# Performance work log

Hardware: AMD Instinct MI355X
Metric: run time of the kernel (lower is better)

Reference implementation:

```python
import jax, jax.numpy as jnp
import numpy as np
from jax import lax

K_NEIGHBORS = 8  # num_neighbors
EPS_BN = 1e-5

def _bn(x, g, b, axes):
    # training-mode batch norm over `axes`, channel axis = 1
    m = jnp.mean(x, axis=axes, keepdims=True)
    v = jnp.var(x, axis=axes, keepdims=True)
    shp = [1] * x.ndim; shp[1] = x.shape[1]
    return (x - m) / jnp.sqrt(v + EPS_BN) * g.reshape(shp) + b.reshape(shp)

def _conv(x, w, b):
    y = lax.conv_general_dilated(x, w, (1, 1), 'SAME',
                                 dimension_numbers=('NCHW', 'OIHW', 'NCHW'))
    return y + b[None, :, None, None]

def setup_inputs() -> dict:
    key = jax.random.key(0)
    ks = jax.random.split(key, 20)
    B, C, H, W = 64, 200, 27, 27
    D, F, NC, HID = 64, 9, 16, 128
    inp = {
        'x': jax.random.normal(ks[0], (B, C, H, W), jnp.float32),
        'conv1_w': jax.random.normal(ks[1], (32, C, 3, 3), jnp.float32) * 0.02,
        'conv1_b': jnp.zeros((32,), jnp.float32),
        'bn1_g': jnp.ones((32,), jnp.float32), 'bn1_b': jnp.zeros((32,), jnp.float32),
        'conv2_w': jax.random.normal(ks[2], (64, 32, 3, 3), jnp.float32) * 0.05,
        'conv2_b': jnp.zeros((64,), jnp.float32),
        'bn2_g': jnp.ones((64,), jnp.float32), 'bn2_b': jnp.zeros((64,), jnp.float32),
        'conv3_w': jax.random.normal(ks[3], (D, 64, 3, 3), jnp.float32) * 0.05,
        'conv3_b': jnp.zeros((D,), jnp.float32),
        'bn3_g': jnp.ones((D,), jnp.float32), 'bn3_b': jnp.zeros((D,), jnp.float32),
        'w_self': jax.random.normal(ks[4], (D, D), jnp.float32) * (2.0 / (2 * D)) ** 0.5,
        'w_nb': jax.random.normal(ks[5], (D, D), jnp.float32) * (2.0 / (2 * D)) ** 0.5,
        'gkan_bias': jnp.zeros((D,), jnp.float32),
        'kan_a': jax.random.normal(ks[6], (D, 3), jnp.float32) * 0.1,
        'kan_b': jax.random.normal(ks[7], (D, 2), jnp.float32) * 0.1,
        'gkan_bn_g': jnp.ones((D,), jnp.float32), 'gkan_bn_b': jnp.zeros((D,), jnp.float32),
        'centers': jax.random.normal(ks[8], (D, F), jnp.float32),
        'gamma': jnp.ones((D, F), jnp.float32) * 0.5,
        'attn_w1': jax.random.normal(ks[9], (D // 4, D), jnp.float32) * 0.1,
        'attn_b1': jnp.zeros((D // 4,), jnp.float32),
        'attn_w2': jax.random.normal(ks[10], (D, D // 4), jnp.float32) * 0.1,
        'attn_b2': jnp.zeros((D,), jnp.float32),
        'fa_bn_g': jnp.ones((D,), jnp.float32), 'fa_bn_b': jnp.zeros((D,), jnp.float32),
        'fc1_w': jax.random.normal(ks[11], (HID, D), jnp.float32) * 0.1,
        'fc1_b': jnp.zeros((HID,), jnp.float32),
        'cls_bn_g': jnp.ones((HID,), jnp.float32), 'cls_bn_b': jnp.zeros((HID,), jnp.float32),
        'fc2_w': jax.random.normal(ks[12], (NC, HID), jnp.float32) * 0.1,
        'fc2_b': jnp.zeros((NC,), jnp.float32),
    }
    return inp

def _forward(x, conv1_w, conv1_b, bn1_g, bn1_b, conv2_w, conv2_b, bn2_g, bn2_b,
             conv3_w, conv3_b, bn3_g, bn3_b, w_self, w_nb, gkan_bias, kan_a, kan_b,
             gkan_bn_g, gkan_bn_b, centers, gamma, attn_w1, attn_b1, attn_w2, attn_b2,
             fa_bn_g, fa_bn_b, fc1_w, fc1_b, cls_bn_g, cls_bn_b, fc2_w, fc2_b):
    # --- CNN encoder ---
    h = jax.nn.relu(_bn(_conv(x, conv1_w, conv1_b), bn1_g, bn1_b, (0, 2, 3)))
    h = jax.nn.relu(_bn(_conv(h, conv2_w, conv2_b), bn2_g, bn2_b, (0, 2, 3)))
    h = jax.nn.relu(_bn(_conv(h, conv3_w, conv3_b), bn3_g, bn3_b, (0, 2, 3)))
    # --- tokenize: [B,D,H,W] -> [B,N,D] ---
    B, D, H, W = h.shape
    N = H * W
    t = h.reshape(B, D, N).transpose(0, 2, 1)
    # --- kNN graph (vectorized topk + scatter) ---
    xx = jnp.sum(t * t, axis=-1, keepdims=True)               # [B,N,1]
    xy = jnp.einsum('bnd,bmd->bnm', t, t)                     # [B,N,N]
    dist = jnp.maximum(xx - 2.0 * xy + xx.transpose(0, 2, 1), 0.0)
    k = min(K_NEIGHBORS + 1, N)
    _, idx = lax.top_k(-dist, k)                              # smallest-k, [B,N,k]
    adj = jnp.zeros((B, N, N), t.dtype).at[
        jnp.arange(B)[:, None, None], jnp.arange(N)[None, :, None], idx[:, :, 1:]
    ].set(1.0)
    deg = jnp.sum(adj, axis=-1) + 1e-6                        # [B,N]
    dinv = deg ** -0.5
    adj_norm = dinv[:, :, None] * adj * dinv[:, None, :] + jnp.eye(N, dtype=t.dtype)[None]
    # --- GKAN graph conv ---
    h_self = t @ w_self                                       # [B,N,D]
    h_nb = jnp.einsum('bnm,bmd->bnd', adj_norm, t @ w_nb)
    g = h_self + h_nb + gkan_bias
    g2 = g * g
    num = kan_a[:, 0] + kan_a[:, 1] * g + kan_a[:, 2] * g2
    den = 1.0 + jnp.abs(kan_b[:, 0] * g + kan_b[:, 1] * g2)
    g = num / (den + 1e-8)
    g = _bn(g.transpose(0, 2, 1), gkan_bn_g, gkan_bn_b, (0, 2)).transpose(0, 2, 1)
    # --- Fuzzy attention (RBF membership; logsumexp(log(v+1e-10)) == sum(v+1e-10)) ---
    d2 = (g[..., None] - centers[None, None]) ** 2            # [B,N,D,F]
    rbf = jnp.sum(jnp.exp(-jnp.abs(gamma)[None, None] * d2) + 1e-10, axis=-1)
    a1 = jax.nn.relu(rbf @ attn_w1.T + attn_b1)
    attn = jax.nn.sigmoid(a1 @ attn_w2.T + attn_b2)
    g = g * attn + g
    g = _bn(g.transpose(0, 2, 1), fa_bn_g, fa_bn_b, (0, 2)).transpose(0, 2, 1)
    # dropout: identity in eval
    # --- global pool + classifier ---
    p = 0.5 * jnp.mean(g, axis=1) + 0.5 * jnp.max(g, axis=1)  # [B,D]
    c = p @ fc1_w.T + fc1_b
    c = jax.nn.relu(_bn(c, cls_bn_g, cls_bn_b, (0,)))
    return c @ fc2_w.T + fc2_b

def reference(x, conv1_w, conv1_b, bn1_g, bn1_b, conv2_w, conv2_b, bn2_g, bn2_b,
              conv3_w, conv3_b, bn3_g, bn3_b, w_self, w_nb, gkan_bias, kan_a, kan_b,
              gkan_bn_g, gkan_bn_b, centers, gamma, attn_w1, attn_b1, attn_w2, attn_b2,
              fa_bn_g, fa_bn_b, fc1_w, fc1_b, cls_bn_g, cls_bn_b, fc2_w, fc2_b):
    return _forward(x, conv1_w, conv1_b, bn1_g, bn1_b, conv2_w, conv2_b, bn2_g, bn2_b,
                    conv3_w, conv3_b, bn3_g, bn3_b, w_self, w_nb, gkan_bias, kan_a, kan_b,
                    gkan_bn_g, gkan_bn_b, centers, gamma, attn_w1, attn_b1, attn_w2, attn_b2,
                    fa_bn_g, fa_bn_b, fc1_w, fc1_b, cls_bn_g, cls_bn_b, fc2_w, fc2_b)
```

## Files before the change

### kernel.cpp

```cpp
#include <hip/hip_runtime.h>
#include <math.h>

#define BATCH 64
#define NTOK  729
#define DIM   64
#define NROWS 46656

#define SROW 33
#define SCH  (29 * SROW)

template<int CIN_CHUNK, bool BN_IN>
__global__ __launch_bounds__(256) void conv3x3_v4(
    const float* __restrict__ in, const float* __restrict__ wgt,
    const float* __restrict__ scsh, float* __restrict__ outp,
    int Cin, int Cout, int cinPerSlab, int nslab)
{
  int bigGroups = Cout / 16;
  int blocksPerB = bigGroups * nslab;
  int b = blockIdx.x / blocksPerB;
  int rr = blockIdx.x % blocksPerB;
  int bg = rr / nslab;
  int slab = rr % nslab;
  int c_begin = slab * cinPerSlab;
  int c_end = c_begin + cinPerSlab; if (c_end > Cin) c_end = Cin;

  __shared__ float s_in[CIN_CHUNK * SCH + SROW];
  __shared__ float s_w[16 * CIN_CHUNK * 12];
  __shared__ float s_sc[CIN_CHUNK];
  __shared__ float s_sh[CIN_CHUNK];

  const int tid = threadIdx.x;
  const int grp = tid >> 7;
  const int idx = tid & 127;
  const bool active = idx < 126;
  const int rp = idx / 9;
  const int py = 2 * rp;
  const int px3 = (idx % 9) * 3;
  const bool row2ok = (py + 1) < 27;

  float acc[8][2][3];
  #pragma unroll
  for (int t = 0; t < 8; ++t)
    #pragma unroll
    for (int rI = 0; rI < 2; ++rI) { acc[t][rI][0]=0.f; acc[t][rI][1]=0.f; acc[t][rI][2]=0.f; }

  const size_t inB = (size_t)b * Cin;

  for (int c0 = c_begin; c0 < c_end; c0 += CIN_CHUNK) {
    int ccn = c_end - c0; if (ccn > CIN_CHUNK) ccn = CIN_CHUNK;
    if (BN_IN && tid < ccn) {
      s_sc[tid] = scsh[c0 + tid];
      s_sh[tid] = scsh[Cin + c0 + tid];
    }
    __syncthreads();
    for (int i = tid; i < CIN_CHUNK * SCH; i += 256) {
      int cc = i / SCH; int r2 = i - cc * SCH; int y = r2 / SROW; int x2 = r2 - y * SROW;
      float v = 0.f;
      if (cc < ccn && y >= 1 && y <= 27 && x2 >= 1 && x2 <= 27) {
        v = in[(inB + (c0 + cc)) * 729 + (y - 1) * 27 + (x2 - 1)];
        if (BN_IN) v = fmaxf(fmaf(v, s_sc[cc], s_sh[cc]), 0.f);
      }
      s_in[i] = v;
    }
    for (int i = tid; i < 16 * CIN_CHUNK * 9; i += 256) {
      int t = i / (CIN_CHUNK * 9); int r2 = i - t * CIN_CHUNK * 9;
      int cc = r2 / 9; int k = r2 - cc * 9;
      float wv = 0.f;
      if (cc < ccn) wv = wgt[((size_t)(bg * 16 + t) * Cin + (c0 + cc)) * 9 + k];
      s_w[(t * CIN_CHUNK + cc) * 12 + k] = wv;
    }
    __syncthreads();
    if (active) {
      #pragma unroll 1
      for (int cc = 0; cc < ccn; ++cc) {
        const float* bp = &s_in[cc * SCH + py * SROW + px3];
        float r0[5], r1[5], r2[5], r3[5];
        #pragma unroll
        for (int j = 0; j < 5; ++j) {
          r0[j] = bp[j];
          r1[j] = bp[SROW + j];
          r2[j] = bp[2*SROW + j];
          r3[j] = bp[3*SROW + j];
        }
        #pragma unroll
        for (int t = 0; t < 8; ++t) {
          const int wb = ((grp * 8 + t) * CIN_CHUNK + cc) * 12;
          const float4 wa = *(const float4*)&s_w[wb];
          const float4 wc = *(const float4*)&s_w[wb + 4];
          const float  w8 = s_w[wb + 8];
          #pragma unroll
          for (int p = 0; p < 3; ++p) {
            acc[t][0][p] += wa.x*r0[p]+wa.y*r0[p+1]+wa.z*r0[p+2]
                          + wa.w*r1[p]+wc.x*r1[p+1]+wc.y*r1[p+2]
                          + wc.z*r2[p]+wc.w*r2[p+1]+w8*r2[p+2];
            acc[t][1][p] += wa.x*r1[p]+wa.y*r1[p+1]+wa.z*r1[p+2]
                          + wa.w*r2[p]+wc.x*r2[p+1]+wc.y*r2[p+2]
                          + wc.z*r3[p]+wc.w*r3[p+1]+w8*r3[p+2];
          }
        }
      }
    }
  }
  if (active) {
    #pragma unroll
    for (int t = 0; t < 8; ++t) {
      size_t base = (((size_t)slab * BATCH + b) * Cout + (bg * 16 + grp * 8 + t)) * 729 + py * 27 + px3;
      outp[base+0]=acc[t][0][0]; outp[base+1]=acc[t][0][1]; outp[base+2]=acc[t][0][2];
      if (row2ok) {
        outp[base+27]=acc[t][1][0]; outp[base+28]=acc[t][1][1]; outp[base+29]=acc[t][1][2];
      }
    }
  }
}

__global__ __launch_bounds__(256) void conv_reduce_stats(
    const float* __restrict__ part, const float* __restrict__ bias,
    float* __restrict__ outp, double* __restrict__ stats, int C, int nslab)
{
  int b = blockIdx.x / C;
  int c = blockIdx.x % C;
  size_t slabStride = (size_t)BATCH * C * 729;
  size_t base = ((size_t)b * C + c) * 729;
  float bv = bias[c];
  float bsum = 0.f, bsq = 0.f;
  for (int e = threadIdx.x; e < 729; e += 256) {
    float v = bv;
    for (int s = 0; s < nslab; ++s) v += part[s*slabStride + base + e];
    outp[base + e] = v;
    bsum += v; bsq += v*v;
  }
  #pragma unroll
  for (int off = 32; off > 0; off >>= 1) {
    bsum += __shfl_down(bsum, off);
    bsq  += __shfl_down(bsq, off);
  }
  __shared__ float rs[4], rq[4];
  int wid = threadIdx.x >> 6;
  if ((threadIdx.x & 63) == 0) { rs[wid] = bsum; rq[wid] = bsq; }
  __syncthreads();
  if (threadIdx.x == 0) {
    float s1 = rs[0]+rs[1]+rs[2]+rs[3];
    float q1 = rq[0]+rq[1]+rq[2]+rq[3];
    atomicAdd(&stats[c], (double)s1);
    atomicAdd(&stats[C + c], (double)q1);
  }
}

__global__ void bn_finalize(const double* __restrict__ stats,
                            const float* __restrict__ gamma, const float* __restrict__ beta,
                            float* __restrict__ scsh, int C, float invCount)
{
  int c = threadIdx.x + blockIdx.x * blockDim.x; if (c >= C) return;
  double mu = stats[c] * (double)invCount;
  double var = stats[C + c] * (double)invCount - mu * mu;
  float rstd = (float)(1.0 / sqrt(var + 1e-5));
  float sc = gamma[c] * rstd;
  scsh[c] = sc;
  scsh[C + c] = beta[c] - (float)mu * sc;
}

__global__ __launch_bounds__(256) void bn_transpose_xx(
    const float* __restrict__ c3, const float* __restrict__ scsh,
    float* __restrict__ t, float* __restrict__ xx)
{
  int lb = (blockIdx.x & 7) * 96 + (blockIdx.x >> 3);
  int b = lb / 12, nt = lb % 12, n0 = nt * 64;
  __shared__ float s[64 * 65];
  for (int i = threadIdx.x; i < 4096; i += 256) {
    int d = i >> 6, j = i & 63; int n = n0 + j;
    float v = 0.f;
    if (n < 729) {
      v = c3[((size_t)b * 64 + d) * 729 + n];
      v = fmaxf(fmaf(v, scsh[d], scsh[64 + d]), 0.f);
    }
    s[d * 65 + j] = v;
  }
  __syncthreads();
  for (int i = threadIdx.x; i < 4096; i += 256) {
    int j = i >> 6, d = i & 63; int n = n0 + j;
    if (n < 729) t[((size_t)b * 729 + n) * 64 + d] = s[d * 65 + j];
  }
  if (threadIdx.x < 64) {
    int j = threadIdx.x; int n = n0 + j;
    if (n < 729) {
      float sm = 0.f;
      #pragma unroll
      for (int d = 0; d < 64; ++d) { float v = s[d * 65 + j]; sm += v * v; }
      xx[b * 729 + n] = sm;
    }
  }
}

__global__ __launch_bounds__(256) void gemm_selfnb(
    const float* __restrict__ t, const float* __restrict__ wself,
    const float* __restrict__ wnb, float* __restrict__ hs, float* __restrict__ hw)
{
  int lb = (blockIdx.x & 7) * 96 + (blockIdx.x >> 3);
  int b = lb / 12, nt = lb % 12, n0 = nt * 64;
  __shared__ __align__(16) float s_tT[64 * 68];
  __shared__ __align__(16) float s_a[64 * 68];
  __shared__ __align__(16) float s_b[64 * 68];
  const int tid = threadIdx.x;
  for (int i = tid; i < 1024; i += 256) {
    int n = i >> 4, dq = i & 15;
    float4 v = make_float4(0.f, 0.f, 0.f, 0.f);
    if (n0 + n < 729) v = *(const float4*)&t[((size_t)b * 729 + n0 + n) * 64 + 4 * dq];
    s_tT[(4*dq+0)*68 + n] = v.x;
    s_tT[(4*dq+1)*68 + n] = v.y;
    s_tT[(4*dq+2)*68 + n] = v.z;
    s_tT[(4*dq+3)*68 + n] = v.w;
  }
  for (int i = tid; i < 1024; i += 256) {
    int d = i >> 4, jq = i & 15;
    *(float4*)&s_a[d*68 + 4*jq] = *(const float4*)&wself[d*64 + 4*jq];
    *(float4*)&s_b[d*68 + 4*jq] = *(const float4*)&wnb[d*64 + 4*jq];
  }
  __syncthreads();
  int ty = tid >> 4, tx = tid & 15;
  float acc0[4][4], acc1[4][4];
  #pragma unroll
  for (int i = 0; i < 4; ++i)
    #pragma unroll
    for (int j = 0; j < 4; ++j) { acc0[i][j] = 0.f; acc1[i][j] = 0.f; }
  #pragma unroll 8
  for (int d = 0; d < 64; ++d) {
    float4 av = *(const float4*)&s_tT[d*68 + 4*ty];
    float4 b1 = *(const float4*)&s_a[d*68 + 4*tx];
    float4 b2 = *(const float4*)&s_b[d*68 + 4*tx];
    float a[4] = {av.x, av.y, av.z, av.w};
    float u[4] = {b1.x, b1.y, b1.z, b1.w};
    float w[4] = {b2.x, b2.y, b2.z, b2.w};
    #pragma unroll
    for (int i = 0; i < 4; ++i)
      #pragma unroll
      for (int j = 0; j < 4; ++j) { acc0[i][j] += a[i]*u[j]; acc1[i][j] += a[i]*w[j]; }
  }
  #pragma unroll
  for (int i = 0; i < 4; ++i) {
    int n = n0 + 4*ty + i;
    if (n < 729) {
      size_t o = ((size_t)b * 729 + n) * 64 + 4*tx;
      *(float4*)&hs[o] = make_float4(acc0[i][0], acc0[i][1], acc0[i][2], acc0[i][3]);
      *(float4*)&hw[o] = make_float4(acc1[i][0], acc1[i][1], acc1[i][2], acc1[i][3]);
    }
  }
}

__global__ __launch_bounds__(256) void dist_topk(
    const float* __restrict__ t, const float* __restrict__ xx, int* __restrict__ nbr)
{
  int lb = (blockIdx.x & 7) * 96 + (blockIdx.x >> 3);
  int b = lb / 12, nt = lb % 12, n0 = nt * 64;
  __shared__ __align__(16) float s_nT[64 * 68];
  __shared__ __align__(16) float s_mT[64 * 68];
  __shared__ __align__(16) float s_S[64 * 68];

  const int tid = threadIdx.x;
  const int ty = tid >> 4, tx = tid & 15;
  const int r = tid & 63, q = tid >> 6;
  const int n_self = n0 + r;
  const size_t tb = (size_t)b * 729;

  float kv[8]; int ki[8];
  #pragma unroll
  for (int i = 0; i < 8; ++i) { kv[i] = 3.0e38f; ki[i] = 0x7fffffff; }

  for (int i = tid; i < 1024; i += 256) {
    int n = i >> 4, dq = i & 15;
    float4 v = make_float4(0.f, 0.f, 0.f, 0.f);
    if (n0 + n < 729) v = *(const float4*)&t[(tb + n0 + n) * 64 + 4 * dq];
    s_nT[(4*dq+0)*68 + n] = v.x;
    s_nT[(4*dq+1)*68 + n] = v.y;
    s_nT[(4*dq+2)*68 + n] = v.z;
    s_nT[(4*dq+3)*68 + n] = v.w;
  }
  for (int i = tid; i < 1024; i += 256) {
    int m = i >> 4, dq = i & 15;
    float4 v = *(const float4*)&t[(tb + m) * 64 + 4 * dq];
    s_mT[(4*dq+0)*68 + m] = v.x;
    s_mT[(4*dq+1)*68 + m] = v.y;
    s_mT[(4*dq+2)*68 + m] = v.z;
    s_mT[(4*dq+3)*68 + m] = v.w;
  }
  __syncthreads();

  for (int mt = 0; mt < 12; ++mt) {
    int m0 = mt * 64;
    float acc[4][4];
    #pragma unroll
    for (int i = 0; i < 4; ++i)
      #pragma unroll
      for (int j = 0; j < 4; ++j) acc[i][j] = 0.f;
    #pragma unroll 8
    for (int d = 0; d < 64; ++d) {
      float4 av4 = *(const float4*)&s_nT[d*68 + 4*ty];
      float4 bv4 = *(const float4*)&s_mT[d*68 + 4*tx];
      float a[4] = {av4.x, av4.y, av4.z, av4.w};
      float bb[4] = {bv4.x, bv4.y, bv4.z, bv4.w};
      #pragma unroll
      for (int i = 0; i < 4; ++i)
        #pragma unroll
        for (int j = 0; j < 4; ++j) acc[i][j] += a[i] * bb[j];
    }
    float xm[4];
    #pragma unroll
    for (int j = 0; j < 4; ++j) {
      int m = m0 + 4*tx + j;
      xm[j] = (m < 729) ? xx[b * 729 + m] : 3.0e38f;
    }
    #pragma unroll
    for (int i = 0; i < 4; ++i) {
      float4 sc = make_float4(fmaf(-2.f, acc[i][0], xm[0]), fmaf(-2.f, acc[i][1], xm[1]),
                              fmaf(-2.f, acc[i][2], xm[2]), fmaf(-2.f, acc[i][3], xm[3]));
      *(float4*)&s_S[(4*ty + i)*68 + 4*tx] = sc;
    }
    __syncthreads();
    if (mt < 11) {
      int m0n = (mt + 1) * 64;
      for (int i = tid; i < 1024; i += 256) {
        int m = i >> 4, dq = i & 15;
        float4 v = make_float4(0.f, 0.f, 0.f, 0.f);
        if (m0n + m < 729) v = *(const float4*)&t[(tb + m0n + m) * 64 + 4 * dq];
        s_mT[(4*dq+0)*68 + m] = v.x;
        s_mT[(4*dq+1)*68 + m] = v.y;
        s_mT[(4*dq+2)*68 + m] = v.z;
        s_mT[(4*dq+3)*68 + m] = v.w;
      }
    }
    #pragma unroll
    for (int c = 0; c < 4; ++c) {
      float4 s4 = *(const float4*)&s_S[r*68 + q*16 + 4*c];
      float sv[4] = {s4.x, s4.y, s4.z, s4.w};
      #pragma unroll
      for (int k = 0; k < 4; ++k) {
        int m = m0 + q*16 + 4*c + k;
        bool valid = (m < 729) && (m != n_self);
        bool lt = valid && ((sv[k] < kv[7]) || (sv[k] == kv[7] && m < ki[7]));
        if (lt) {
          float cv = sv[k]; int ci = m;
          #pragma unroll
          for (int ii = 0; ii < 8; ++ii) {
            bool less = (cv < kv[ii]) || (cv == kv[ii] && ci < ki[ii]);
            float tv = less ? kv[ii] : cv; int ti = less ? ki[ii] : ci;
            kv[ii] = less ? cv : kv[ii]; ki[ii] = less ? ci : ki[ii];
            cv = tv; ci = ti;
          }
        }
      }
    }
    __syncthreads();
  }
  float* mv = s_mT;
  int*   mi = (int*)s_nT;
  #pragma unroll
  for (int i2 = 0; i2 < 8; ++i2) { mv[r*33 + q*8 + i2] = kv[i2]; mi[r*33 + q*8 + i2] = ki[i2]; }
  __syncthreads();
  if (tid < 64) {
    int n = n0 + tid;
    if (n < 729) {
      int rb = tid * 33;
      int p0 = 0, p1 = 0, p2 = 0, p3 = 0;
      int* op = &nbr[((size_t)b * 729 + n) * 8];
      for (int o = 0; o < 8; ++o) {
        float bvv = 3.5e38f; int bii = 0x7fffffff; int bq = 0;
        {
          float v = mv[rb + 0*8 + p0]; int ii = mi[rb + 0*8 + p0];
          if (v < bvv || (v == bvv && ii < bii)) { bvv = v; bii = ii; bq = 0; }
        }
        {
          float v = mv[rb + 1*8 + p1]; int ii = mi[rb + 1*8 + p1];
          if (v < bvv || (v == bvv && ii < bii)) { bvv = v; bii = ii; bq = 1; }
        }
        {
          float v = mv[rb + 2*8 + p2]; int ii = mi[rb + 2*8 + p2];
          if (v < bvv || (v == bvv && ii < bii)) { bvv = v; bii = ii; bq = 2; }
        }
        {
          float v = mv[rb + 3*8 + p3]; int ii = mi[rb + 3*8 + p3];
          if (v < bvv || (v == bvv && ii < bii)) { bvv = v; bii = ii; bq = 3; }
        }
        p0 += (bq == 0); p1 += (bq == 1); p2 += (bq == 2); p3 += (bq == 3);
        op[o] = bii;
      }
    }
  }
}

__global__ __launch_bounds__(256) void gkan_kernel(
    const float* __restrict__ hs, const float* __restrict__ hw,
    const int* __restrict__ nbr, const float* __restrict__ bias,
    const float* __restrict__ kan_a, const float* __restrict__ kan_b,
    float* __restrict__ gpre)
{
  int row = blockIdx.x * 4 + (threadIdx.x >> 6);
  int d = threadIdx.x & 63;
  float degf = 8.0f + 1e-6f;
  float coef = 1.0f / degf;
  size_t bbase = (size_t)(row / 729) * 729;
  float v = hs[(size_t)row * 64 + d] + hw[(size_t)row * 64 + d] + bias[d];
  float nsum = 0.f;
  #pragma unroll
  for (int j = 0; j < 8; ++j) {
    int m = nbr[(size_t)row * 8 + j];
    nsum += hw[(bbase + m) * 64 + d];
  }
  v += coef * nsum;
  float a0 = kan_a[d*3], a1 = kan_a[d*3+1], a2 = kan_a[d*3+2];
  float b0 = kan_b[d*2], b1 = kan_b[d*2+1];
  float v2 = v * v;
  float num = a0 + a1*v + a2*v2;
  float den = 1.f + fabsf(b0*v + b1*v2);
  gpre[(size_t)row * 64 + d] = num / (den + 1e-8f);
}

__global__ __launch_bounds__(256) void stats_tok(
    const float* __restrict__ g, double* __restrict__ stats)
{
  int d = threadIdx.x & 63, qq = threadIdx.x >> 6;
  int r0 = blockIdx.x * 183;
  int rend = r0 + 183; if (rend > NROWS) rend = NROWS;
  float sm = 0.f, sq = 0.f;
  for (int r = r0 + qq; r < rend; r += 4) {
    float v = g[(size_t)r * 64 + d];
    sm += v; sq += v * v;
  }
  __shared__ float ls[256], lq[256];
  ls[threadIdx.x] = sm; lq[threadIdx.x] = sq;
  __syncthreads();
  if (threadIdx.x < 64) {
    sm = ls[d] + ls[64+d] + ls[128+d] + ls[192+d];
    sq = lq[d] + lq[64+d] + lq[128+d] + lq[192+d];
    atomicAdd(&stats[d], (double)sm);
    atomicAdd(&stats[64 + d], (double)sq);
  }
}

__global__ __launch_bounds__(256) void fuzzy_attn(
    const float* __restrict__ gpre, const float* __restrict__ scshG,
    const float* __restrict__ centers, const float* __restrict__ gam,
    const float* __restrict__ w1, const float* __restrict__ b1,
    const float* __restrict__ w2, const float* __restrict__ b2,
    float* __restrict__ g2)
{
  int wv = threadIdx.x >> 6, d = threadIdx.x & 63;
  int row = blockIdx.x * 4 + wv;
  __shared__ float s_rbf[4][64];
  __shared__ float s_a1[4][16];
  float v = gpre[(size_t)row * 64 + d];
  float gn = fmaf(v, scshG[d], scshG[64 + d]);
  float acc = 0.f;
  #pragma unroll
  for (int f = 0; f < 9; ++f) {
    float dc = gn - centers[d*9 + f];
    acc += expf(-fabsf(gam[d*9 + f]) * dc * dc);
  }
  s_rbf[wv][d] = acc + 9e-10f;
  __syncthreads();
  if (d < 16) {
    float a = b1[d];
    #pragma unroll 8
    for (int k = 0; k < 64; ++k) a += w1[d*64 + k] * s_rbf[wv][k];
    s_a1[wv][d] = fmaxf(a, 0.f);
  }
  __syncthreads();
  float a2 = b2[d];
  #pragma unroll
  for (int i = 0; i < 16; ++i) a2 += w2[d*16 + i] * s_a1[wv][i];
  float sig = 1.f / (1.f + expf(-a2));
  g2[(size_t)row * 64 + d] = gn * (1.f + sig);
}

__global__ __launch_bounds__(256) void pool_kernel(
    const float* __restrict__ g2, const float* __restrict__ scshF, float* __restrict__ p)
{
  int b = blockIdx.x;
  int d = threadIdx.x & 63, qq = threadIdx.x >> 6;
  float sc = scshF[d], sh = scshF[64 + d];
  float sm = 0.f, mx = -3.0e38f;
  for (int n = qq; n < 729; n += 4) {
    float v = fmaf(g2[((size_t)b * 729 + n) * 64 + d], sc, sh);
    sm += v; mx = fmaxf(mx, v);
  }
  __shared__ float ls[256], lm[256];
  ls[threadIdx.x] = sm; lm[threadIdx.x] = mx;
  __syncthreads();
  if (threadIdx.x < 64) {
    sm = ls[d] + ls[64+d] + ls[128+d] + ls[192+d];
    mx = fmaxf(fmaxf(lm[d], lm[64+d]), fmaxf(lm[128+d], lm[192+d]));
    p[b * 64 + d] = 0.5f * (sm / 729.f) + 0.5f * mx;
  }
}

__global__ __launch_bounds__(256) void classifier(
    const float* __restrict__ p, const float* __restrict__ f1w, const float* __restrict__ f1b,
    const float* __restrict__ bng, const float* __restrict__ bnb,
    const float* __restrict__ f2w, const float* __restrict__ f2b, float* __restrict__ outp)
{
  __shared__ float s_p[64 * 64];
  __shared__ float s_c[64 * 128];
  __shared__ float s_sc[128], s_sh[128];
  for (int i = threadIdx.x; i < 4096; i += 256) s_p[i] = p[i];
  __syncthreads();
  for (int o = threadIdx.x; o < 8192; o += 256) {
    int b = o >> 7, h = o & 127;
    float acc = f1b[h];
    #pragma unroll 8
    for (int d = 0; d < 64; ++d) acc += s_p[b*64 + d] * f1w[h*64 + d];
    s_c[o] = acc;
  }
  __syncthreads();
  if (threadIdx.x < 128) {
    int h = threadIdx.x;
    float sm = 0.f, sq = 0.f;
    for (int b = 0; b < 64; ++b) { float v = s_c[b*128 + h]; sm += v; sq += v*v; }
    float mu = sm / 64.f;
    float var = sq / 64.f - mu * mu;
    float rstd = rsqrtf(var + 1e-5f);
    float sc = bng[h] * rstd;
    s_sc[h] = sc; s_sh[h] = bnb[h] - mu * sc;
  }
  __syncthreads();
  for (int o = threadIdx.x; o < 1024; o += 256) {
    int b = o >> 4, j = o & 15;
    float acc = f2b[j];
    #pragma unroll 8
    for (int h = 0; h < 128; ++h) {
      float v = fmaxf(fmaf(s_c[b*128 + h], s_sc[h], s_sh[h]), 0.f);
      acc += f2w[j*128 + h] * v;
    }
    outp[o] = acc;
  }
}

extern "C" void kernel_launch(void* const* d_in, const int* in_sizes, int n_in,
                              void* d_out, int out_size, void* d_ws, size_t ws_size,
                              hipStream_t stream)
{
  const float* x      = (const float*)d_in[0];
  const float* c1w    = (const float*)d_in[1];
  const float* c1b    = (const float*)d_in[2];
  const float* bn1g   = (const float*)d_in[3];
  const float* bn1b   = (const float*)d_in[4];
  const float* c2wt   = (const float*)d_in[5];
  const float* c2b    = (const float*)d_in[6];
  const float* bn2g   = (const float*)d_in[7];
  const float* bn2b   = (const float*)d_in[8];
  const float* c3wt   = (const float*)d_in[9];
  const float* c3b    = (const float*)d_in[10];
  const float* bn3g   = (const float*)d_in[11];
  const float* bn3b   = (const float*)d_in[12];
  const float* wself  = (const float*)d_in[13];
  const float* wnb    = (const float*)d_in[14];
  const float* gbias  = (const float*)d_in[15];
  const float* kana   = (const float*)d_in[16];
  const float* kanb   = (const float*)d_in[17];
  const float* gbng   = (const float*)d_in[18];
  const float* gbnb   = (const float*)d_in[19];
  const float* cent   = (const float*)d_in[20];
  const float* gamr   = (const float*)d_in[21];
  const float* aw1    = (const float*)d_in[22];
  const float* ab1    = (const float*)d_in[23];
  const float* aw2    = (const float*)d_in[24];
  const float* ab2    = (const float*)d_in[25];
  const float* fbng   = (const float*)d_in[26];
  const float* fbnb   = (const float*)d_in[27];
  const float* f1w    = (const float*)d_in[28];
  const float* f1b    = (const float*)d_in[29];
  const float* cbng   = (const float*)d_in[30];
  const float* cbnb   = (const float*)d_in[31];
  const float* f2w    = (const float*)d_in[32];
  const float* f2b    = (const float*)d_in[33];

  char* ws = (char*)d_ws;
  float*  P     = (float*) (ws + 0);
  float*  c1    = (float*) (ws + 23887872);
  float*  c2    = (float*) (ws + 29859840);
  float*  c3    = (float*) (ws + 41803776);
  int*    nbr   = (int*)   (ws + 53747712);
  float*  xx    = (float*) (ws + 55240704);
  double* stats = (double*)(ws + 55427328);
  float*  scsh  = (float*) (ws + 55431936);
  float*  pbuf  = (float*) (ws + 55434240);
  float* hw   = P;
  float* t    = (float*)(ws + 11943936);
  float* hs   = c2;
  float* gpre = c3;
  float* g2   = t;

  hipMemsetAsync(stats, 0, 576 * sizeof(double), stream);

  const float inv = 1.0f / 46656.0f;

  conv3x3_v4<8,false><<<dim3(512), dim3(256), 0, stream>>>(
      x,  c1w, nullptr, P, 200, 32, 50, 4);
  conv_reduce_stats<<<dim3(2048), dim3(256), 0, stream>>>(P, c1b, c1, stats, 32, 4);
  bn_finalize<<<dim3(1), dim3(32), 0, stream>>>(stats, bn1g, bn1b, scsh, 32, inv);
  conv3x3_v4<8,true><<<dim3(512), dim3(256), 0, stream>>>(
      c1, c2wt, scsh, P, 32, 64, 16, 2);
  conv_reduce_stats<<<dim3(4096), dim3(256), 0, stream>>>(P, c2b, c2, stats + 64, 64, 2);
  bn_finalize<<<dim3(1), dim3(64), 0, stream>>>(stats + 64, bn2g, bn2b, scsh + 64, 64, inv);
  conv3x3_v4<8,true><<<dim3(512), dim3(256), 0, stream>>>(
      c2, c3wt, scsh + 64, P, 64, 64, 32, 2);
  conv_reduce_stats<<<dim3(4096), dim3(256), 0, stream>>>(P, c3b, c3, stats + 192, 64, 2);
  bn_finalize<<<dim3(1), dim3(64), 0, stream>>>(stats + 192, bn3g, bn3b, scsh + 192, 64, inv);
  bn_transpose_xx<<<dim3(768), dim3(256), 0, stream>>>(c3, scsh + 192, t, xx);
  gemm_selfnb<<<dim3(768), dim3(256), 0, stream>>>(t, wself, wnb, hs, hw);
  dist_topk<<<dim3(768), dim3(256), 0, stream>>>(t, xx, nbr);
  gkan_kernel<<<dim3(11664), dim3(256), 0, stream>>>(hs, hw, nbr, gbias, kana, kanb, gpre);
  stats_tok<<<dim3(256), dim3(256), 0, stream>>>(gpre, stats + 320);
  bn_finalize<<<dim3(1), dim3(64), 0, stream>>>(stats + 320, gbng, gbnb, scsh + 320, 64, inv);
  fuzzy_attn<<<dim3(11664), dim3(256), 0, stream>>>(gpre, scsh + 320, cent, gamr, aw1, ab1, aw2, ab2, g2);
  stats_tok<<<dim3(256), dim3(256), 0, stream>>>(g2, stats + 448);
  bn_finalize<<<dim3(1), dim3(64), 0, stream>>>(stats + 448, fbng, fbnb, scsh + 448, 64, inv);
  pool_kernel<<<dim3(64), dim3(256), 0, stream>>>(g2, scsh + 448, pbuf);
  classifier<<<dim3(1), dim3(256), 0, stream>>>(pbuf, f1w, f1b, cbng, cbnb, f2w, f2b, (float*)d_out);
}
```

Measured before the change: 885.6 us.

## Restructure dist_topk with register-tiled distances and double buffering; shrink conv blocks

In dist_topk, each thread now owns two query rows and eight candidate columns, and keeps a top-8 per row in registers. This removes the shared score matrix and its round-trip through shared memory. The candidate tile is double-buffered, with the next tile prefetched into registers during compute, and the final merge now combines eight partial lists per row instead of four. Separately, the conv kernel drops from 256-thread blocks covering 16 output channels to 128-thread blocks covering 8 channels with twice the grid. That raises block count but halves input-tile reuse across channels.

Measured after the change: 1.030 ms. +16.3%, slower.

```diff
diff --git a/kernel.cpp b/kernel.cpp
--- a/kernel.cpp
+++ b/kernel.cpp
@@ -10,32 +10,30 @@
 #define SCH  (29 * SROW)
 
 template<int CIN_CHUNK, bool BN_IN>
-__global__ __launch_bounds__(256) void conv3x3_v4(
+__global__ __launch_bounds__(128) void conv3x3_v5(
     const float* __restrict__ in, const float* __restrict__ wgt,
     const float* __restrict__ scsh, float* __restrict__ outp,
     int Cin, int Cout, int cinPerSlab, int nslab)
 {
-  int bigGroups = Cout / 16;
-  int blocksPerB = bigGroups * nslab;
+  int groups = Cout / 8;
+  int blocksPerB = groups * nslab;
   int b = blockIdx.x / blocksPerB;
   int rr = blockIdx.x % blocksPerB;
-  int bg = rr / nslab;
+  int g = rr / nslab;
   int slab = rr % nslab;
   int c_begin = slab * cinPerSlab;
   int c_end = c_begin + cinPerSlab; if (c_end > Cin) c_end = Cin;
 
   __shared__ float s_in[CIN_CHUNK * SCH + SROW];
-  __shared__ float s_w[16 * CIN_CHUNK * 12];
+  __shared__ float s_w[8 * CIN_CHUNK * 12];
   __shared__ float s_sc[CIN_CHUNK];
   __shared__ float s_sh[CIN_CHUNK];
 
   const int tid = threadIdx.x;
-  const int grp = tid >> 7;
-  const int idx = tid & 127;
-  const bool active = idx < 126;
-  const int rp = idx / 9;
+  const bool active = tid < 126;
+  const int rp = tid / 9;
   const int py = 2 * rp;
-  const int px3 = (idx % 9) * 3;
+  const int px3 = (tid % 9) * 3;
   const bool row2ok = (py + 1) < 27;
 
   float acc[8][2][3];
@@ -53,7 +51,7 @@
       s_sh[tid] = scsh[Cin + c0 + tid];
     }
     __syncthreads();
-    for (int i = tid; i < CIN_CHUNK * SCH; i += 256) {
+    for (int i = tid; i < CIN_CHUNK * SCH; i += 128) {
       int cc = i / SCH; int r2 = i - cc * SCH; int y = r2 / SROW; int x2 = r2 - y * SROW;
       float v = 0.f;
       if (cc < ccn && y >= 1 && y <= 27 && x2 >= 1 && x2 <= 27) {
@@ -62,11 +60,11 @@
       }
       s_in[i] = v;
     }
-    for (int i = tid; i < 16 * CIN_CHUNK * 9; i += 256) {
+    for (int i = tid; i < 8 * CIN_CHUNK * 9; i += 128) {
       int t = i / (CIN_CHUNK * 9); int r2 = i - t * CIN_CHUNK * 9;
       int cc = r2 / 9; int k = r2 - cc * 9;
       float wv = 0.f;
-      if (cc < ccn) wv = wgt[((size_t)(bg * 16 + t) * Cin + (c0 + cc)) * 9 + k];
+      if (cc < ccn) wv = wgt[((size_t)(g * 8 + t) * Cin + (c0 + cc)) * 9 + k];
       s_w[(t * CIN_CHUNK + cc) * 12 + k] = wv;
     }
     __syncthreads();
@@ -84,7 +82,7 @@
         }
         #pragma unroll
         for (int t = 0; t < 8; ++t) {
-          const int wb = ((grp * 8 + t) * CIN_CHUNK + cc) * 12;
+          const int wb = (t * CIN_CHUNK + cc) * 12;
           const float4 wa = *(const float4*)&s_w[wb];
           const float4 wc = *(const float4*)&s_w[wb + 4];
           const float  w8 = s_w[wb + 8];
@@ -104,7 +102,7 @@
   if (active) {
     #pragma unroll
     for (int t = 0; t < 8; ++t) {
-      size_t base = (((size_t)slab * BATCH + b) * Cout + (bg * 16 + grp * 8 + t)) * 729 + py * 27 + px3;
+      size_t base = (((size_t)slab * BATCH + b) * Cout + (g * 8 + t)) * 729 + py * 27 + px3;
       outp[base+0]=acc[t][0][0]; outp[base+1]=acc[t][0][1]; outp[base+2]=acc[t][0][2];
       if (row2ok) {
         outp[base+27]=acc[t][1][0]; outp[base+28]=acc[t][1][1]; outp[base+29]=acc[t][1][2];
@@ -252,18 +250,23 @@
   int lb = (blockIdx.x & 7) * 96 + (blockIdx.x >> 3);
   int b = lb / 12, nt = lb % 12, n0 = nt * 64;
   __shared__ __align__(16) float s_nT[64 * 68];
-  __shared__ __align__(16) float s_mT[64 * 68];
-  __shared__ __align__(16) float s_S[64 * 68];
+  __shared__ __align__(16) float s_m0[64 * 68];
+  __shared__ __align__(16) float s_m1[64 * 68];
 
   const int tid = threadIdx.x;
-  const int ty = tid >> 4, tx = tid & 15;
-  const int r = tid & 63, q = tid >> 6;
-  const int n_self = n0 + r;
+  const int rg = tid >> 3;
+  const int cg = tid & 7;
+  const int r0 = 2 * rg, r1 = r0 + 1;
+  const int self0 = n0 + r0, self1 = n0 + r1;
   const size_t tb = (size_t)b * 729;
-
-  float kv[8]; int ki[8];
-  #pragma unroll
-  for (int i = 0; i < 8; ++i) { kv[i] = 3.0e38f; ki[i] = 0x7fffffff; }
+  const float* xxb = &xx[b * 729];
+
+  float kv0[8], kv1[8]; int ki0[8], ki1[8];
+  #pragma unroll
+  for (int i = 0; i < 8; ++i) {
+    kv0[i] = 3.0e38f; ki0[i] = 0x7fffffff;
+    kv1[i] = 3.0e38f; ki1[i] = 0x7fffffff;
+  }
 
   for (int i = tid; i < 1024; i += 256) {
     int n = i >> 4, dq = i & 15;
@@ -277,109 +280,122 @@
   for (int i = tid; i < 1024; i += 256) {
     int m = i >> 4, dq = i & 15;
     float4 v = *(const float4*)&t[(tb + m) * 64 + 4 * dq];
-    s_mT[(4*dq+0)*68 + m] = v.x;
-    s_mT[(4*dq+1)*68 + m] = v.y;
-    s_mT[(4*dq+2)*68 + m] = v.z;
-    s_mT[(4*dq+3)*68 + m] = v.w;
+    s_m0[(4*dq+0)*68 + m] = v.x;
+    s_m0[(4*dq+1)*68 + m] = v.y;
+    s_m0[(4*dq+2)*68 + m] = v.z;
+    s_m0[(4*dq+3)*68 + m] = v.w;
   }
   __syncthreads();
 
   for (int mt = 0; mt < 12; ++mt) {
-    int m0 = mt * 64;
-    float acc[4][4];
+    const int m0 = mt * 64;
+    const float* cur = (mt & 1) ? s_m1 : s_m0;
+    float*       nxt = (mt & 1) ? s_m0 : s_m1;
+
+    float4 st[4];
+    if (mt < 11) {
+      #pragma unroll
+      for (int j = 0; j < 4; ++j) {
+        int i = tid + 256 * j; int m = i >> 4, dq = i & 15;
+        int mm = m0 + 64 + m;
+        st[j] = (mm < 729) ? *(const float4*)&t[(tb + mm) * 64 + 4 * dq]
+                           : make_float4(0.f, 0.f, 0.f, 0.f);
+      }
+    }
+    float xm[8];
     #pragma unroll
-    for (int i = 0; i < 4; ++i)
+    for (int k = 0; k < 8; ++k) {
+      xm[k] = xxb[m0 + 8*cg + k];
+    }
+
+    float acc0[8], acc1[8];
+    #pragma unroll
+    for (int j = 0; j < 8; ++j) { acc0[j] = 0.f; acc1[j] = 0.f; }
+    #pragma unroll 4
+    for (int d = 0; d < 64; ++d) {
+      float2 a  = *(const float2*)&s_nT[d*68 + r0];
+      float4 bA = *(const float4*)&cur[d*68 + 8*cg];
+      float4 bB = *(const float4*)&cur[d*68 + 8*cg + 4];
+      float bb[8] = {bA.x, bA.y, bA.z, bA.w, bB.x, bB.y, bB.z, bB.w};
       #pragma unroll
-      for (int j = 0; j < 4; ++j) acc[i][j] = 0.f;
-    #pragma unroll 8
-    for (int d = 0; d < 64; ++d) {
-      float4 av4 = *(const float4*)&s_nT[d*68 + 4*ty];
-      float4 bv4 = *(const float4*)&s_mT[d*68 + 4*tx];
-      float a[4] = {av4.x, av4.y, av4.z, av4.w};
-      float bb[4] = {bv4.x, bv4.y, bv4.z, bv4.w};
-      #pragma unroll
-      for (int i = 0; i < 4; ++i)
-        #pragma unroll
-        for (int j = 0; j < 4; ++j) acc[i][j] += a[i] * bb[j];
-    }
-    float xm[4];
+      for (int j = 0; j < 8; ++j) {
+        acc0[j] += a.x * bb[j];
+        acc1[j] += a.y * bb[j];
+      }
+    }
+
     #pragma unroll
-    for (int j = 0; j < 4; ++j) {
-      int m = m0 + 4*tx + j;
-      xm[j] = (m < 729) ? xx[b * 729 + m] : 3.0e38f;
-    }
-    #pragma unroll
-    for (int i = 0; i < 4; ++i) {
-      float4 sc = make_float4(fmaf(-2.f, acc[i][0], xm[0]), fmaf(-2.f, acc[i][1], xm[1]),
-                              fmaf(-2.f, acc[i][2], xm[2]), fmaf(-2.f, acc[i][3], xm[3]));
-      *(float4*)&s_S[(4*ty + i)*68 + 4*tx] = sc;
-    }
-    __syncthreads();
-    if (mt < 11) {
-      int m0n = (mt + 1) * 64;
-      for (int i = tid; i < 1024; i += 256) {
-        int m = i >> 4, dq = i & 15;
-        float4 v = make_float4(0.f, 0.f, 0.f, 0.f);
-        if (m0n + m < 729) v = *(const float4*)&t[(tb + m0n + m) * 64 + 4 * dq];
-        s_mT[(4*dq+0)*68 + m] = v.x;
-        s_mT[(4*dq+1)*68 + m] = v.y;
-        s_mT[(4*dq+2)*68 + m] = v.z;
-        s_mT[(4*dq+3)*68 + m] = v.w;
-      }
-    }
-    #pragma unroll
-    for (int c = 0; c < 4; ++c) {
-      float4 s4 = *(const float4*)&s_S[r*68 + q*16 + 4*c];
-      float sv[4] = {s4.x, s4.y, s4.z, s4.w};
-      #pragma unroll
-      for (int k = 0; k < 4; ++k) {
-        int m = m0 + q*16 + 4*c + k;
-        bool valid = (m < 729) && (m != n_self);
-        bool lt = valid && ((sv[k] < kv[7]) || (sv[k] == kv[7] && m < ki[7]));
+    for (int k = 0; k < 8; ++k) {
+      int m = m0 + 8*cg + k;
+      bool inb = (m < 729);
+      {
+        float sv = fmaf(-2.f, acc0[k], xm[k]);
+        bool lt = inb && (m != self0) &&
+                  ((sv < kv0[7]) || (sv == kv0[7] && m < ki0[7]));
         if (lt) {
-          float cv = sv[k]; int ci = m;
+          float cv = sv; int ci = m;
           #pragma unroll
           for (int ii = 0; ii < 8; ++ii) {
-            bool less = (cv < kv[ii]) || (cv == kv[ii] && ci < ki[ii]);
-            float tv = less ? kv[ii] : cv; int ti = less ? ki[ii] : ci;
-            kv[ii] = less ? cv : kv[ii]; ki[ii] = less ? ci : ki[ii];
+            bool less = (cv < kv0[ii]) || (cv == kv0[ii] && ci < ki0[ii]);
+            float tv = less ? kv0[ii] : cv; int ti = less ? ki0[ii] : ci;
+            kv0[ii] = less ? cv : kv0[ii]; ki0[ii] = less ? ci : ki0[ii];
             cv = tv; ci = ti;
           }
         }
       }
+      {
+        float sv = fmaf(-2.f, acc1[k], xm[k]);
+        bool lt = inb && (m != self1) &&
+                  ((sv < kv1[7]) || (sv == kv1[7] && m < ki1[7]));
+        if (lt) {
+          float cv = sv; int ci = m;
+          #pragma unroll
+          for (int ii = 0; ii < 8; ++ii) {
+            bool less = (cv < kv1[ii]) || (cv == kv1[ii] && ci < ki1[ii]);
+            float tv = less ? kv1[ii] : cv; int ti = less ? ki1[ii] : ci;
+            kv1[ii] = less ? cv : kv1[ii]; ki1[ii] = less ? ci : ki1[ii];
+            cv = tv; ci = ti;
+          }
+        }
+      }
+    }
+
+    if (mt < 11) {
+      #pragma unroll
+      for (int j = 0; j < 4; ++j) {
+        int i = tid + 256 * j; int m = i >> 4, dq = i & 15;
+        nxt[(4*dq+0)*68 + m] = st[j].x;
+        nxt[(4*dq+1)*68 + m] = st[j].y;
+        nxt[(4*dq+2)*68 + m] = st[j].z;
+        nxt[(4*dq+3)*68 + m] = st[j].w;
+      }
     }
     __syncthreads();
   }
-  float* mv = s_mT;
-  int*   mi = (int*)s_nT;
-  #pragma unroll
-  for (int i2 = 0; i2 < 8; ++i2) { mv[r*33 + q*8 + i2] = kv[i2]; mi[r*33 + q*8 + i2] = ki[i2]; }
+
+  float* mv = s_m0;
+  int*   mi = (int*)s_m1;
+  #pragma unroll
+  for (int k = 0; k < 8; ++k) {
+    mv[r0*68 + cg*8 + k] = kv0[k]; mi[r0*68 + cg*8 + k] = ki0[k];
+    mv[r1*68 + cg*8 + k] = kv1[k]; mi[r1*68 + cg*8 + k] = ki1[k];
+  }
   __syncthreads();
   if (tid < 64) {
     int n = n0 + tid;
     if (n < 729) {
-      int rb = tid * 33;
-      int p0 = 0, p1 = 0, p2 = 0, p3 = 0;
+      int rb = tid * 68;
+      int p[8] = {0,0,0,0,0,0,0,0};
       int* op = &nbr[((size_t)b * 729 + n) * 8];
       for (int o = 0; o < 8; ++o) {
         float bvv = 3.5e38f; int bii = 0x7fffffff; int bq = 0;
-        {
-          float v = mv[rb + 0*8 + p0]; int ii = mi[rb + 0*8 + p0];
-          if (v < bvv || (v == bvv && ii < bii)) { bvv = v; bii = ii; bq = 0; }
+        #pragma unroll
+        for (int q = 0; q < 8; ++q) {
+          float v = mv[rb + q*8 + p[q]]; int ii = mi[rb + q*8 + p[q]];
+          if (v < bvv || (v == bvv && ii < bii)) { bvv = v; bii = ii; bq = q; }
         }
-        {
-          float v = mv[rb + 1*8 + p1]; int ii = mi[rb + 1*8 + p1];
-          if (v < bvv || (v == bvv && ii < bii)) { bvv = v; bii = ii; bq = 1; }
-        }
-        {
-          float v = mv[rb + 2*8 + p2]; int ii = mi[rb + 2*8 + p2];
-          if (v < bvv || (v == bvv && ii < bii)) { bvv = v; bii = ii; bq = 2; }
-        }
-        {
-          float v = mv[rb + 3*8 + p3]; int ii = mi[rb + 3*8 + p3];
-          if (v < bvv || (v == bvv && ii < bii)) { bvv = v; bii = ii; bq = 3; }
-        }
-        p0 += (bq == 0); p1 += (bq == 1); p2 += (bq == 2); p3 += (bq == 3);
+        #pragma unroll
+        for (int q = 0; q < 8; ++q) p[q] += (bq == q);
         op[o] = bii;
       }
     }
@@ -591,15 +607,15 @@
 
   const float inv = 1.0f / 46656.0f;
 
-  conv3x3_v4<8,false><<<dim3(512), dim3(256), 0, stream>>>(
+  conv3x3_v5<8,false><<<dim3(1024), dim3(128), 0, stream>>>(
       x,  c1w, nullptr, P, 200, 32, 50, 4);
   conv_reduce_stats<<<dim3(2048), dim3(256), 0, stream>>>(P, c1b, c1, stats, 32, 4);
   bn_finalize<<<dim3(1), dim3(32), 0, stream>>>(stats, bn1g, bn1b, scsh, 32, inv);
-  conv3x3_v4<8,true><<<dim3(512), dim3(256), 0, stream>>>(
+  conv3x3_v5<8,true><<<dim3(1024), dim3(128), 0, stream>>>(
       c1, c2wt, scsh, P, 32, 64, 16, 2);
   conv_reduce_stats<<<dim3(4096), dim3(256), 0, stream>>>(P, c2b, c2, stats + 64, 64, 2);
   bn_finalize<<<dim3(1), dim3(64), 0, stream>>>(stats + 64, bn2g, bn2b, scsh + 64, 64, inv);
-  conv3x3_v4<8,true><<<dim3(512), dim3(256), 0, stream>>>(
+  conv3x3_v5<8,true><<<dim3(1024), dim3(128), 0, stream>>>(
       c2, c3wt, scsh + 64, P, 64, 64, 32, 2);
   conv_reduce_stats<<<dim3(4096), dim3(256), 0, stream>>>(P, c3b, c3, stats + 192, 64, 2);
   bn_finalize<<<dim3(1), dim3(64), 0, stream>>>(stats + 192, bn3g, bn3b, scsh + 192, 64, inv);
```
